# Optimization experiments

Measured on AMD Instinct MI355X. Metric: run time of the kernel, lower is better.

The kernel has to match this reference:

```python
import jax, jax.numpy as jnp
import numpy as np

LEVEL = 3
NUM_BANDS = LEVEL + 1
B, N, D_MODEL, PATCH_NUMS, PRED_LEN = 32, 7, 768, 64, 336

# db4 lowpass decomposition filter (pywt convention)
_DB4_DEC_LO = np.array([
    -0.010597401784997278, 0.032883011666982945, 0.030841381835986965,
    -0.18703481171888114, -0.02798376941698385, 0.6308807679295904,
    0.7148465705525415, 0.23037781330885523], dtype=np.float32)
REC_LO = _DB4_DEC_LO[::-1].copy()                                   # reconstruction lowpass
REC_HI = (_DB4_DEC_LO * ((-1.0) ** (np.arange(8) + 1))).astype(np.float32)  # reconstruction highpass (QMF)


def _upsample2(x):
    # zero-interleave along last axis: (..., L) -> (..., 2L)
    z = jnp.zeros_like(x)
    return jnp.stack([x, z], axis=-1).reshape(*x.shape[:-1], 2 * x.shape[-1])


def _idwt_per(ca, cd, rec_lo, rec_hi):
    # single-level inverse DWT, periodization mode, along last axis: (..., L) -> (..., 2L)
    F = rec_lo.shape[0]
    ua, ud = _upsample2(ca), _upsample2(cd)
    y = jnp.zeros_like(ua)
    for k in range(F):  # small fixed tap loop (F=8)
        y = y + jnp.roll(ua, k, axis=-1) * rec_lo[k] + jnp.roll(ud, k, axis=-1) * rec_hi[k]
    return jnp.roll(y, -(F // 2 - 1), axis=-1)  # compensate filter delay


def _iswt(coeffs, level, rec_lo, rec_hi):
    # coeffs: (..., T, level+1) with bands ordered [cA, cD_level, ..., cD1]
    T = coeffs.shape[-2]
    out = coeffs[..., 0]
    for j in range(level, 0, -1):
        step = 2 ** (j - 1)
        cd = coeffs[..., level - j + 1]
        M = T // step
        # gather the `step` interleaved subsequences as a batch axis: (..., step, M)
        o = jnp.moveaxis(out.reshape(*out.shape[:-1], M, step), -1, -2)
        d = jnp.moveaxis(cd.reshape(*cd.shape[:-1], M, step), -1, -2)
        x1 = _idwt_per(o[..., 0::2], d[..., 0::2], rec_lo, rec_hi)
        x2 = jnp.roll(_idwt_per(o[..., 1::2], d[..., 1::2], rec_lo, rec_hi), 1, axis=-1)
        new = 0.5 * (x1 + x2)  # (..., step, M)
        out = jnp.moveaxis(new, -2, -1).reshape(*out.shape[:-1], T)
    return out


def setup_inputs() -> dict:
    key = jax.random.key(0)
    kx, kw, kb = jax.random.split(key, 3)
    Din = D_MODEL * PATCH_NUMS
    x = jax.random.normal(kx, (B, N, D_MODEL, PATCH_NUMS), dtype=jnp.float32)
    # Linear init ~ U(-1/sqrt(Din), 1/sqrt(Din)); small normal is equivalent for a reference
    W = jax.random.normal(kw, (NUM_BANDS, Din, PRED_LEN), dtype=jnp.float32) * (1.0 / np.sqrt(Din))
    b = jax.random.normal(kb, (NUM_BANDS, PRED_LEN), dtype=jnp.float32) * 0.01
    return {"x": x, "W": W, "b": b}


def reference(x, W, b):
    # x: (B, N, d_model, patch_nums); W: (bands, d_model*patch_nums, pred_len); b: (bands, pred_len)
    Bb, Nn, dm, P = x.shape
    xf = x.reshape(Bb, Nn, dm * P)  # Flatten(start_dim=-2)
    # all band projections as one batched GEMM -> (B, N, pred_len, bands)
    coeffs = jnp.einsum('bnd,kdp->bnpk', xf, W) + b.T
    rec_lo = jnp.asarray(REC_LO)
    rec_hi = jnp.asarray(REC_HI)
    return _iswt(coeffs, LEVEL, rec_lo, rec_hi)  # (B, N, pred_len)
```

## Files before the change

### kernel.cpp

```cpp
#include <hip/hip_runtime.h>
#include <stdint.h>

#define M_ROWS   224
#define K_DIM    49152
#define NCOL     1344
#define PRED     336
#define S_CHUNKS 48
#define STEPS    32

#define XB_OFFSET (32u * 1024u * 1024u)

typedef __attribute__((ext_vector_type(8))) short short8;
typedef __attribute__((ext_vector_type(4))) float floatx4;

__device__ __forceinline__ uint16_t f32_to_bf16(float f) {
    uint32_t u = __builtin_bit_cast(uint32_t, f);
    uint32_t r = (u + 0x7fffu + ((u >> 16) & 1u)) >> 16;
    return (uint16_t)r;
}
__device__ __forceinline__ float bf16_to_f32(uint16_t h) {
    uint32_t u = ((uint32_t)h) << 16;
    return __builtin_bit_cast(float, u);
}
__device__ __forceinline__ uint32_t pack2(float lo, float hi) {
    return (uint32_t)f32_to_bf16(lo) | ((uint32_t)f32_to_bf16(hi) << 16);
}

__global__ __launch_bounds__(256) void cvt_x(
    const float* __restrict__ X, uint16_t* __restrict__ Xb)
{
    const size_t i = ((size_t)blockIdx.x * 256 + threadIdx.x) * 8;
    const float4 a = *(const float4*)(X + i);
    const float4 b = *(const float4*)(X + i + 4);
    uint4 o;
    o.x = pack2(a.x, a.y);
    o.y = pack2(a.z, a.w);
    o.z = pack2(b.x, b.y);
    o.w = pack2(b.z, b.w);
    *(uint4*)(Xb + i) = o;
}

__global__ __launch_bounds__(256, 4) void gemm_partial(
    const uint16_t* __restrict__ Xb,
    const float* __restrict__ W,
    uint16_t* __restrict__ P)
{
    __shared__ uint16_t lA[2][14 * 512];

    const int id = blockIdx.x;
    const int g  = id & 7;
    const int q  = id >> 3;
    const int ct = q % 21;
    const int s  = g + 8 * (q / 21);

    const int tid  = threadIdx.x;
    const int lane = tid & 63;
    const int w    = tid >> 6;
    const int l15  = lane & 15;
    const int kq   = lane >> 4;
    const int c0w  = ct * 64 + w * 16;
    const int band = c0w / PRED;
    const int p0   = c0w - band * PRED;

    const float* wbase = W + (size_t)band * ((size_t)K_DIM * PRED)
                           + (size_t)(kq * 8) * PRED
                           + (size_t)(p0 + l15);
    const size_t grow = (size_t)l15 * K_DIM + (size_t)kq * 8;
    const int kbase = s * (STEPS * 32);

    floatx4 acc[14];
    #pragma unroll
    for (int f = 0; f < 14; ++f) acc[f] = (floatx4){0.f, 0.f, 0.f, 0.f};

    float wA[8], wB[8];

    #pragma unroll
    for (int t = 0; t < 4; ++t) {
        const int f = w + 4 * t;
        if (f < 14) {
            const uint16_t* gp = Xb + (size_t)(16 * f) * K_DIM + grow + kbase;
            __builtin_amdgcn_global_load_lds(
                (const __attribute__((address_space(1))) void*)gp,
                (__attribute__((address_space(3))) void*)&lA[0][f * 512],
                16, 0, 0);
        }
    }
    #pragma unroll
    for (int j = 0; j < 8; ++j) wA[j] = wbase[(size_t)(kbase + j) * PRED];
    #pragma unroll
    for (int j = 0; j < 8; ++j) wB[j] = wbase[(size_t)(kbase + 32 + j) * PRED];
    asm volatile("s_waitcnt vmcnt(16)" ::: "memory");
    __builtin_amdgcn_s_barrier();
    __builtin_amdgcn_sched_barrier(0);

#define GEMM_STEP(WREG, RBUF, WBUF, ST)                                        \
    {                                                                          \
        short8 bfrag;                                                          \
        _Pragma("unroll")                                                      \
        for (int j = 0; j < 4; ++j)                                            \
            ((uint32_t*)&bfrag)[j] = pack2(WREG[2*j], WREG[2*j+1]);            \
        if ((ST) + 1 < STEPS) {                                                \
            const int kx = kbase + ((ST) + 1) * 32;                            \
            _Pragma("unroll")                                                  \
            for (int t = 0; t < 4; ++t) {                                      \
                const int f = w + 4 * t;                                       \
                if (f < 14) {                                                  \
                    const uint16_t* gp = Xb + (size_t)(16 * f) * K_DIM + grow + kx; \
                    __builtin_amdgcn_global_load_lds(                          \
                        (const __attribute__((address_space(1))) void*)gp,     \
                        (__attribute__((address_space(3))) void*)&lA[WBUF][f * 512], \
                        16, 0, 0);                                             \
                }                                                              \
            }                                                                  \
        }                                                                      \
        if ((ST) + 2 < STEPS) {                                                \
            const int kw2 = kbase + ((ST) + 2) * 32;                           \
            _Pragma("unroll")                                                  \
            for (int j = 0; j < 8; ++j)                                        \
                WREG[j] = wbase[(size_t)(kw2 + j) * PRED];                     \
        }                                                                      \
        _Pragma("unroll")                                                      \
        for (int f = 0; f < 14; ++f) {                                         \
            short8 afrag = *(const short8*)&lA[RBUF][f * 512 + lane * 8];      \
            acc[f] = __builtin_amdgcn_mfma_f32_16x16x32_bf16(                  \
                afrag, bfrag, acc[f], 0, 0, 0);                                \
        }                                                                      \
        asm volatile("s_waitcnt vmcnt(8) lgkmcnt(0)" ::: "memory");            \
        __builtin_amdgcn_s_barrier();                                          \
        __builtin_amdgcn_sched_barrier(0);                                     \
    }

    for (int st = 0; st < STEPS; st += 2) {
        GEMM_STEP(wA, 0, 1, st)
        GEMM_STEP(wB, 1, 0, st + 1)
    }
#undef GEMM_STEP

    const int col = c0w + l15;
    #pragma unroll
    for (int f = 0; f < 14; ++f) {
        #pragma unroll
        for (int r = 0; r < 4; ++r) {
            const int m = 16 * f + kq * 4 + r;
            P[((size_t)m * S_CHUNKS + s) * NCOL + col] = f32_to_bf16(acc[f][r]);
        }
    }
}

__device__ const float REC_LO[8] = {
     0.23037781330885523f,  0.7148465705525415f,   0.6308807679295904f,
    -0.02798376941698385f, -0.18703481171888114f,  0.030841381835986965f,
     0.032883011666982945f, -0.010597401784997278f };
__device__ const float REC_HI[8] = {
     0.010597401784997278f, 0.032883011666982945f, -0.030841381835986965f,
    -0.18703481171888114f,  0.02798376941698385f,   0.6308807679295904f,
    -0.7148465705525415f,   0.23037781330885523f };

__global__ __launch_bounds__(1024) void reduce_iswt(
    const uint16_t* __restrict__ P,
    const float* __restrict__ bias,
    float* __restrict__ out)
{
    __shared__ float coeff[NCOL];
    __shared__ float buf[2][PRED];

    const int row = blockIdx.x;
    const int tid = threadIdx.x;
    const uint32_t* pr = (const uint32_t*)(P + (size_t)row * S_CHUNKS * NCOL);

    if (tid < NCOL / 2) {
        float a0 = 0.f, a1 = 0.f;
        #pragma unroll 8
        for (int s = 0; s < S_CHUNKS; ++s) {
            const uint32_t v = pr[s * (NCOL / 2) + tid];
            a0 += bf16_to_f32((uint16_t)(v & 0xffff));
            a1 += bf16_to_f32((uint16_t)(v >> 16));
        }
        coeff[2 * tid]     = a0 + bias[2 * tid];
        coeff[2 * tid + 1] = a1 + bias[2 * tid + 1];
    }
    __syncthreads();

    if (tid < PRED) buf[0][tid] = coeff[tid];
    __syncthreads();

    int curb = 0;
    for (int j = 3; j >= 1; --j) {
        const int step = 1 << (j - 1);
        const int M    = PRED / step;
        const float* cd  = &coeff[(4 - j) * PRED];
        const float* cur = buf[curb];
        float* nxt       = buf[curb ^ 1];
        if (tid < PRED) {
            const int t = tid;
            const int sidx = t & (step - 1);
            const int m = t / step;
            const int mm1 = (m == 0) ? (M - 1) : (m - 1);
            float x1 = 0.f, x2 = 0.f;
            #pragma unroll
            for (int k = 0; k < 8; ++k) {
                int i1 = m + 3 - k;  if (i1 < 0) i1 += M; else if (i1 >= M) i1 -= M;
                if ((i1 & 1) == 0) {
                    const int pos = i1 * step + sidx;
                    x1 += cur[pos] * REC_LO[k] + cd[pos] * REC_HI[k];
                }
                int i2 = mm1 + 3 - k;  if (i2 < 0) i2 += M; else if (i2 >= M) i2 -= M;
                if ((i2 & 1) == 0) {
                    const int pos = (i2 + 1) * step + sidx;
                    x2 += cur[pos] * REC_LO[k] + cd[pos] * REC_HI[k];
                }
            }
            nxt[t] = 0.5f * (x1 + x2);
        }
        __syncthreads();
        curb ^= 1;
    }

    if (tid < PRED) out[(size_t)row * PRED + tid] = buf[curb][tid];
}

extern "C" void kernel_launch(void* const* d_in, const int* in_sizes, int n_in,
                              void* d_out, int out_size, void* d_ws, size_t ws_size,
                              hipStream_t stream) {
    const float* X    = (const float*)d_in[0];
    const float* W    = (const float*)d_in[1];
    const float* bias = (const float*)d_in[2];
    float* out        = (float*)d_out;
    uint16_t* P       = (uint16_t*)d_ws;
    uint16_t* Xb      = (uint16_t*)((char*)d_ws + XB_OFFSET);

    cvt_x       <<<5376, 256, 0, stream>>>(X, Xb);
    gemm_partial<<<21 * S_CHUNKS, 256, 0, stream>>>(Xb, W, P);
    reduce_iswt <<<M_ROWS, 1024, 0, stream>>>(P, bias, out);
}
```

Before: 429.2 us.

## Stage W tiles through LDS with async loads and triple buffering

Replaces per-lane strided scalar global loads of the fp32 weight matrix with 16-byte global_load_lds transfers into a per-wave, triple-buffered LDS tile. B fragments are then read from LDS, and the prefetch distance is two steps ahead. The split-K partition changes from 48 chunks of 32 steps to 32 chunks of 48 steps, which reduces the partial-sum output and the reduction work. Occupancy hint drops from 4 to 3 blocks per CU because of the extra LDS, and the wait counts are hand-tuned, so getting them wrong risks races.

```diff
diff --git a/kernel.cpp b/kernel.cpp
--- a/kernel.cpp
+++ b/kernel.cpp
@@ -5,8 +5,8 @@
 #define K_DIM    49152
 #define NCOL     1344
 #define PRED     336
-#define S_CHUNKS 48
-#define STEPS    32
+#define S_CHUNKS 32
+#define STEPS    48
 
 #define XB_OFFSET (32u * 1024u * 1024u)
 
@@ -40,12 +40,13 @@
     *(uint4*)(Xb + i) = o;
 }
 
-__global__ __launch_bounds__(256, 4) void gemm_partial(
+__global__ __launch_bounds__(256, 3) void gemm_partial(
     const uint16_t* __restrict__ Xb,
     const float* __restrict__ W,
     uint16_t* __restrict__ P)
 {
-    __shared__ uint16_t lA[2][14 * 512];
+    __shared__ uint16_t lX[2][14 * 512];
+    __shared__ float    lW[4][3][512];
 
     const int id = blockIdx.x;
     const int g  = id & 7;
@@ -62,17 +63,15 @@
     const int band = c0w / PRED;
     const int p0   = c0w - band * PRED;
 
-    const float* wbase = W + (size_t)band * ((size_t)K_DIM * PRED)
-                           + (size_t)(kq * 8) * PRED
-                           + (size_t)(p0 + l15);
+    const float* wsrc = W + (size_t)band * ((size_t)K_DIM * PRED)
+                          + (size_t)(lane >> 2) * PRED
+                          + (size_t)(p0 + (lane & 3) * 4);
     const size_t grow = (size_t)l15 * K_DIM + (size_t)kq * 8;
     const int kbase = s * (STEPS * 32);
 
     floatx4 acc[14];
     #pragma unroll
     for (int f = 0; f < 14; ++f) acc[f] = (floatx4){0.f, 0.f, 0.f, 0.f};
-
-    float wA[8], wB[8];
 
     #pragma unroll
     for (int t = 0; t < 4; ++t) {
@@ -81,59 +80,85 @@
             const uint16_t* gp = Xb + (size_t)(16 * f) * K_DIM + grow + kbase;
             __builtin_amdgcn_global_load_lds(
                 (const __attribute__((address_space(1))) void*)gp,
-                (__attribute__((address_space(3))) void*)&lA[0][f * 512],
+                (__attribute__((address_space(3))) void*)&lX[0][f * 512],
                 16, 0, 0);
         }
     }
     #pragma unroll
-    for (int j = 0; j < 8; ++j) wA[j] = wbase[(size_t)(kbase + j) * PRED];
-    #pragma unroll
-    for (int j = 0; j < 8; ++j) wB[j] = wbase[(size_t)(kbase + 32 + j) * PRED];
-    asm volatile("s_waitcnt vmcnt(16)" ::: "memory");
+    for (int b = 0; b < 2; ++b) {
+        #pragma unroll
+        for (int i = 0; i < 2; ++i) {
+            const float* gp = wsrc + (size_t)(kbase + b * 32 + i * 16) * PRED;
+            __builtin_amdgcn_global_load_lds(
+                (const __attribute__((address_space(1))) void*)gp,
+                (__attribute__((address_space(3))) void*)&lW[w][b][i * 256],
+                16, 0, 0);
+        }
+    }
+    asm volatile("s_waitcnt vmcnt(2)" ::: "memory");
     __builtin_amdgcn_s_barrier();
     __builtin_amdgcn_sched_barrier(0);
 
-#define GEMM_STEP(WREG, RBUF, WBUF, ST)                                        \
+#define GEMM_STEP(ST, XR, XW, WR, WW, DO_X, DO_W, WAITSTR)                     \
     {                                                                          \
-        short8 bfrag;                                                          \
-        _Pragma("unroll")                                                      \
-        for (int j = 0; j < 4; ++j)                                            \
-            ((uint32_t*)&bfrag)[j] = pack2(WREG[2*j], WREG[2*j+1]);            \
-        if ((ST) + 1 < STEPS) {                                                \
+        if (DO_X) {                                                            \
             const int kx = kbase + ((ST) + 1) * 32;                            \
             _Pragma("unroll")                                                  \
             for (int t = 0; t < 4; ++t) {                                      \
                 const int f = w + 4 * t;                                       \
                 if (f < 14) {                                                  \
-                    const uint16_t* gp = Xb + (size_t)(16 * f) * K_DIM + grow + kx; \
+                    const uint16_t* gp = Xb + (size_t)(16*f)*K_DIM + grow + kx;\
                     __builtin_amdgcn_global_load_lds(                          \
                         (const __attribute__((address_space(1))) void*)gp,     \
-                        (__attribute__((address_space(3))) void*)&lA[WBUF][f * 512], \
+                        (__attribute__((address_space(3))) void*)&lX[XW][f*512],\
                         16, 0, 0);                                             \
                 }                                                              \
             }                                                                  \
         }                                                                      \
-        if ((ST) + 2 < STEPS) {                                                \
+        if (DO_W) {                                                            \
             const int kw2 = kbase + ((ST) + 2) * 32;                           \
             _Pragma("unroll")                                                  \
-            for (int j = 0; j < 8; ++j)                                        \
-                WREG[j] = wbase[(size_t)(kw2 + j) * PRED];                     \
+            for (int i = 0; i < 2; ++i) {                                      \
+                const float* gp = wsrc + (size_t)(kw2 + i * 16) * PRED;        \
+                __builtin_amdgcn_global_load_lds(                              \
+                    (const __attribute__((address_space(1))) void*)gp,         \
+                    (__attribute__((address_space(3))) void*)&lW[w][WW][i*256],\
+                    16, 0, 0);                                                 \
+            }                                                                  \
         }                                                                      \
+        float wv[8];                                                           \
+        _Pragma("unroll")                                                      \
+        for (int j = 0; j < 8; ++j)                                            \
+            wv[j] = lW[w][WR][(kq * 8 + j) * 16 + l15];                        \
+        short8 bfrag;                                                          \
+        _Pragma("unroll")                                                      \
+        for (int j = 0; j < 4; ++j)                                            \
+            ((uint32_t*)&bfrag)[j] = pack2(wv[2 * j], wv[2 * j + 1]);          \
         _Pragma("unroll")                                                      \
         for (int f = 0; f < 14; ++f) {                                         \
-            short8 afrag = *(const short8*)&lA[RBUF][f * 512 + lane * 8];      \
+            short8 afrag = *(const short8*)&lX[XR][f * 512 + lane * 8];        \
             acc[f] = __builtin_amdgcn_mfma_f32_16x16x32_bf16(                  \
                 afrag, bfrag, acc[f], 0, 0, 0);                                \
         }                                                                      \
-        asm volatile("s_waitcnt vmcnt(8) lgkmcnt(0)" ::: "memory");            \
+        asm volatile("s_waitcnt " WAITSTR " lgkmcnt(0)" ::: "memory");         \
         __builtin_amdgcn_s_barrier();                                          \
         __builtin_amdgcn_sched_barrier(0);                                     \
     }
 
-    for (int st = 0; st < STEPS; st += 2) {
-        GEMM_STEP(wA, 0, 1, st)
-        GEMM_STEP(wB, 1, 0, st + 1)
-    }
+    for (int st = 0; st < 42; st += 6) {
+        GEMM_STEP(st + 0, 0, 1, 0, 2, 1, 1, "vmcnt(2)")
+        GEMM_STEP(st + 1, 1, 0, 1, 0, 1, 1, "vmcnt(2)")
+        GEMM_STEP(st + 2, 0, 1, 2, 1, 1, 1, "vmcnt(2)")
+        GEMM_STEP(st + 3, 1, 0, 0, 2, 1, 1, "vmcnt(2)")
+        GEMM_STEP(st + 4, 0, 1, 1, 0, 1, 1, "vmcnt(2)")
+        GEMM_STEP(st + 5, 1, 0, 2, 1, 1, 1, "vmcnt(2)")
+    }
+    GEMM_STEP(42, 0, 1, 0, 2, 1, 1, "vmcnt(2)")
+    GEMM_STEP(43, 1, 0, 1, 0, 1, 1, "vmcnt(2)")
+    GEMM_STEP(44, 0, 1, 2, 1, 1, 1, "vmcnt(2)")
+    GEMM_STEP(45, 1, 0, 0, 2, 1, 1, "vmcnt(2)")
+    GEMM_STEP(46, 0, 1, 1, 0, 1, 0, "vmcnt(0)")
+    GEMM_STEP(47, 1, 0, 2, 1, 0, 0, "vmcnt(0)")
 #undef GEMM_STEP
 
     const int col = c0w + l15;
```

Measured after the change: 432.6 us. No clear change (+0.8%).

## Triple-buffer X tiles in LDS with two-step-ahead prefetch

Applied to the files above, without the earlier changes.

Moves the GEMM's LDS staging of the bf16 X tiles from double to triple buffering and prefetches them two k-steps ahead instead of one, matching the existing W register prefetch distance. Wait counts are adjusted so each step waits only on its own tile's loads. The aim is to hide more global load latency behind the MFMA work. In exchange it uses more LDS per block, and launch bounds drop from 4 to 3 blocks per SIMD, which lowers occupancy.

```diff
diff --git a/kernel.cpp b/kernel.cpp
--- a/kernel.cpp
+++ b/kernel.cpp
@@ -40,12 +40,12 @@
     *(uint4*)(Xb + i) = o;
 }
 
-__global__ __launch_bounds__(256, 4) void gemm_partial(
+__global__ __launch_bounds__(256, 3) void gemm_partial(
     const uint16_t* __restrict__ Xb,
     const float* __restrict__ W,
     uint16_t* __restrict__ P)
 {
-    __shared__ uint16_t lA[2][14 * 512];
+    __shared__ uint16_t lX[3][14 * 512];
 
     const int id = blockIdx.x;
     const int g  = id & 7;
@@ -75,45 +75,49 @@
     float wA[8], wB[8];
 
     #pragma unroll
-    for (int t = 0; t < 4; ++t) {
-        const int f = w + 4 * t;
-        if (f < 14) {
-            const uint16_t* gp = Xb + (size_t)(16 * f) * K_DIM + grow + kbase;
-            __builtin_amdgcn_global_load_lds(
-                (const __attribute__((address_space(1))) void*)gp,
-                (__attribute__((address_space(3))) void*)&lA[0][f * 512],
-                16, 0, 0);
+    for (int b = 0; b < 2; ++b) {
+        #pragma unroll
+        for (int t = 0; t < 4; ++t) {
+            const int f = w + 4 * t;
+            if (f < 14) {
+                const uint16_t* gp = Xb + (size_t)(16 * f) * K_DIM + grow
+                                        + kbase + b * 32;
+                __builtin_amdgcn_global_load_lds(
+                    (const __attribute__((address_space(1))) void*)gp,
+                    (__attribute__((address_space(3))) void*)&lX[b][f * 512],
+                    16, 0, 0);
+            }
         }
     }
     #pragma unroll
     for (int j = 0; j < 8; ++j) wA[j] = wbase[(size_t)(kbase + j) * PRED];
     #pragma unroll
     for (int j = 0; j < 8; ++j) wB[j] = wbase[(size_t)(kbase + 32 + j) * PRED];
-    asm volatile("s_waitcnt vmcnt(16)" ::: "memory");
+    asm volatile("s_waitcnt vmcnt(0)" ::: "memory");
     __builtin_amdgcn_s_barrier();
     __builtin_amdgcn_sched_barrier(0);
 
-#define GEMM_STEP(WREG, RBUF, WBUF, ST)                                        \
+#define GEMM_STEP(ST, XR, XW, WREG, DO_PRE, WAITSTR)                           \
     {                                                                          \
+        if (DO_PRE) {                                                          \
+            const int kx = kbase + ((ST) + 2) * 32;                            \
+            _Pragma("unroll")                                                  \
+            for (int t = 0; t < 4; ++t) {                                      \
+                const int f = w + 4 * t;                                       \
+                if (f < 14) {                                                  \
+                    const uint16_t* gp = Xb + (size_t)(16*f)*K_DIM + grow + kx;\
+                    __builtin_amdgcn_global_load_lds(                          \
+                        (const __attribute__((address_space(1))) void*)gp,     \
+                        (__attribute__((address_space(3))) void*)&lX[XW][f*512],\
+                        16, 0, 0);                                             \
+                }                                                              \
+            }                                                                  \
+        }                                                                      \
         short8 bfrag;                                                          \
         _Pragma("unroll")                                                      \
         for (int j = 0; j < 4; ++j)                                            \
             ((uint32_t*)&bfrag)[j] = pack2(WREG[2*j], WREG[2*j+1]);            \
-        if ((ST) + 1 < STEPS) {                                                \
-            const int kx = kbase + ((ST) + 1) * 32;                            \
-            _Pragma("unroll")                                                  \
-            for (int t = 0; t < 4; ++t) {                                      \
-                const int f = w + 4 * t;                                       \
-                if (f < 14) {                                                  \
-                    const uint16_t* gp = Xb + (size_t)(16 * f) * K_DIM + grow + kx; \
-                    __builtin_amdgcn_global_load_lds(                          \
-                        (const __attribute__((address_space(1))) void*)gp,     \
-                        (__attribute__((address_space(3))) void*)&lA[WBUF][f * 512], \
-                        16, 0, 0);                                             \
-                }                                                              \
-            }                                                                  \
-        }                                                                      \
-        if ((ST) + 2 < STEPS) {                                                \
+        if (DO_PRE) {                                                          \
             const int kw2 = kbase + ((ST) + 2) * 32;                           \
             _Pragma("unroll")                                                  \
             for (int j = 0; j < 8; ++j)                                        \
@@ -121,19 +125,25 @@
         }                                                                      \
         _Pragma("unroll")                                                      \
         for (int f = 0; f < 14; ++f) {                                         \
-            short8 afrag = *(const short8*)&lA[RBUF][f * 512 + lane * 8];      \
+            short8 afrag = *(const short8*)&lX[XR][f * 512 + lane * 8];        \
             acc[f] = __builtin_amdgcn_mfma_f32_16x16x32_bf16(                  \
                 afrag, bfrag, acc[f], 0, 0, 0);                                \
         }                                                                      \
-        asm volatile("s_waitcnt vmcnt(8) lgkmcnt(0)" ::: "memory");            \
+        asm volatile("s_waitcnt " WAITSTR " lgkmcnt(0)" ::: "memory");         \
         __builtin_amdgcn_s_barrier();                                          \
         __builtin_amdgcn_sched_barrier(0);                                     \
     }
 
-    for (int st = 0; st < STEPS; st += 2) {
-        GEMM_STEP(wA, 0, 1, st)
-        GEMM_STEP(wB, 1, 0, st + 1)
-    }
+    for (int st = 0; st < 30; st += 6) {
+        GEMM_STEP(st + 0, 0, 2, wA, 1, "vmcnt(11)")
+        GEMM_STEP(st + 1, 1, 0, wB, 1, "vmcnt(11)")
+        GEMM_STEP(st + 2, 2, 1, wA, 1, "vmcnt(11)")
+        GEMM_STEP(st + 3, 0, 2, wB, 1, "vmcnt(11)")
+        GEMM_STEP(st + 4, 1, 0, wA, 1, "vmcnt(11)")
+        GEMM_STEP(st + 5, 2, 1, wB, 1, "vmcnt(11)")
+    }
+    GEMM_STEP(30, 0, 2, wA, 0, "vmcnt(0)")
+    GEMM_STEP(31, 1, 0, wB, 0, "vmcnt(0)")
 #undef GEMM_STEP
 
     const int col = c0w + l15;
```

After: 428.4 us. No clear change (-0.2%).
